# Optimization experiments

Measured on AMD Instinct MI355X. Metric: run time of the kernel, lower is better.

Reference implementation:

```python
import jax, jax.numpy as jnp
import numpy as np


def setup_inputs() -> dict:
    key = jax.random.key(0)
    kx, kb, kc, ka, kd = jax.random.split(key, 5)
    B, L, D, N = 8, 4096, 1024, 128
    x = jax.random.normal(kx, (B, L, D), jnp.float32)
    B_w = jax.random.normal(kb, (N, D), jnp.float32) * 0.01  # nn.Linear(d_model->d_state).weight
    C_w = jax.random.normal(kc, (D, N), jnp.float32)         # nn.Linear(d_state->d_model).weight
    # stable negative log_A (HiPPO init gives -|diag|+0.1 < 0)
    log_A = -jax.random.uniform(ka, (N,), jnp.float32) * 3.0 - 0.1
    D_param = jax.random.normal(kd, (D,), jnp.float32)
    return dict(x=x, B_w=B_w, C_w=C_w, log_A=log_A, D_param=D_param)


def reference(x, B_w, C_w, log_A, D_param):
    # x: (B,L,D); B_w: (N,D); C_w: (D,N); log_A: (N,); D_param: (D,)
    A = jnp.exp(log_A)                                   # (N,) diagonal transition
    x_proj = jnp.einsum('bld,nd->bln', x, B_w)           # B @ x  -> (B,L,N)

    def step(h, u):                                      # h_t = A*h_{t-1} + u_t
        h = A * h + u
        return h, h

    h0 = jnp.zeros((x.shape[0], B_w.shape[0]), x.dtype)  # (B,N)
    _, hs = jax.lax.scan(step, h0, jnp.swapaxes(x_proj, 0, 1))  # hs: (L,B,N)

    y = jnp.einsum('lbn,dn->bld', hs, C_w)               # C @ h -> (B,L,D)
    y = y + x * D_param                                  # skip term D*x

    last = x_proj[:, -1, :]                              # (B,N)
    final_state = jnp.broadcast_to(last.mean(axis=0, keepdims=True), last.shape)
    return y, final_state
```

## Files before the change

### kernel.cpp

```cpp
#include <hip/hip_runtime.h>


typedef _Float16 half8 __attribute__((ext_vector_type(8)));
typedef float f32x4 __attribute__((ext_vector_type(4)));

#define BDIM 8
#define LDIM 4096
#define DDIM 1024
#define NDIM 128
#define MTOT (BDIM * LDIM)
#define CHUNK 128
#define NCHUNK (LDIM / CHUNK)
#define TOTCHUNK (BDIM * NCHUNK)

__global__ __launch_bounds__(256) void gemm1(const float* __restrict__ x,
                                             const float* __restrict__ Bw,
                                             float* __restrict__ xp) {
    __shared__ _Float16 As[128 * 32];
    __shared__ _Float16 Bs[128 * 32];
    const int t = threadIdx.x;
    const int row0 = blockIdx.x * 128;
    const int wave = t >> 6, lane = t & 63;
    const int wr = (wave >> 1) * 64, wc = (wave & 1) * 64;
    const int lrow = lane & 15, kq = (lane >> 4) * 8;

    f32x4 acc[4][4] = {};

    for (int kk = 0; kk < 1024; kk += 32) {
#pragma unroll
        for (int j = 0; j < 4; ++j) {
            int i = t + 256 * j;
            int r = i >> 3, c4 = i & 7;
            float4 v = *reinterpret_cast<const float4*>(&x[(row0 + r) * 1024 + kk + c4 * 4]);
            _Float16* dst = &As[r * 32 + c4 * 4];
            dst[0] = (_Float16)v.x; dst[1] = (_Float16)v.y;
            dst[2] = (_Float16)v.z; dst[3] = (_Float16)v.w;
        }
#pragma unroll
        for (int j = 0; j < 4; ++j) {
            int i = t + 256 * j;
            int r = i >> 3, c4 = i & 7;
            float4 v = *reinterpret_cast<const float4*>(&Bw[r * 1024 + kk + c4 * 4]);
            _Float16* dst = &Bs[r * 32 + c4 * 4];
            dst[0] = (_Float16)v.x; dst[1] = (_Float16)v.y;
            dst[2] = (_Float16)v.z; dst[3] = (_Float16)v.w;
        }
        __syncthreads();

        half8 bf[4];
#pragma unroll
        for (int ct = 0; ct < 4; ++ct)
            bf[ct] = *reinterpret_cast<const half8*>(&Bs[(wc + ct * 16 + lrow) * 32 + kq]);
#pragma unroll
        for (int rt = 0; rt < 4; ++rt) {
            half8 af = *reinterpret_cast<const half8*>(&As[(wr + rt * 16 + lrow) * 32 + kq]);
#pragma unroll
            for (int ct = 0; ct < 4; ++ct)
                acc[rt][ct] = __builtin_amdgcn_mfma_f32_16x16x32_f16(af, bf[ct], acc[rt][ct], 0, 0, 0);
        }
        __syncthreads();
    }

    const int q4 = (lane >> 4) * 4;
#pragma unroll
    for (int rt = 0; rt < 4; ++rt) {
#pragma unroll
        for (int ct = 0; ct < 4; ++ct) {
            int col = wc + ct * 16 + lrow;
#pragma unroll
            for (int i = 0; i < 4; ++i)
                xp[(row0 + wr + rt * 16 + q4 + i) * 128 + col] = acc[rt][ct][i];
        }
    }
}

__global__ void scan_agg(const float* __restrict__ xp, const float* __restrict__ logA,
                         float* __restrict__ agg) {
    const int chunk = blockIdx.x;
    const int n = threadIdx.x;
    const float A = expf(logA[n]);
    const float* u = xp + chunk * CHUNK * 128 + n;
    float h = 0.f;
#pragma unroll 4
    for (int j = 0; j < CHUNK; ++j)
        h = fmaf(A, h, u[j * 128]);
    agg[chunk * 128 + n] = h;
}

__global__ void scan_carry(const float* __restrict__ agg, const float* __restrict__ logA,
                           float* __restrict__ hprev) {
    const int idx = blockIdx.x * blockDim.x + threadIdx.x;
    const int b = idx >> 7, n = idx & 127;
    const float A128 = expf(128.f * logA[n]);
    float c = 0.f;
    for (int ch = 0; ch < NCHUNK; ++ch) {
        int g = (b * NCHUNK + ch) * 128 + n;
        hprev[g] = c;
        c = fmaf(A128, c, agg[g]);
    }
}

__global__ void scan_final(const float* __restrict__ xp, const float* __restrict__ logA,
                           const float* __restrict__ hprev, _Float16* __restrict__ hs) {
    const int chunk = blockIdx.x;
    const int n = threadIdx.x;
    const float A = expf(logA[n]);
    float h = hprev[chunk * 128 + n];
    const float* u = xp + chunk * CHUNK * 128 + n;
    _Float16* o = hs + chunk * CHUNK * 128 + n;
#pragma unroll 4
    for (int j = 0; j < CHUNK; ++j) {
        h = fmaf(A, h, u[j * 128]);
        o[j * 128] = (_Float16)h;
    }
}

__global__ __launch_bounds__(256) void gemm2(const _Float16* __restrict__ hs,
                                             const float* __restrict__ Cw,
                                             const float* __restrict__ x,
                                             const float* __restrict__ Dp,
                                             float* __restrict__ y) {
    __shared__ _Float16 As[128 * 32];
    __shared__ _Float16 Bs[128 * 32];
    const int t = threadIdx.x;
    const int row0 = blockIdx.x * 128;
    const int col0 = blockIdx.y * 128;
    const int wave = t >> 6, lane = t & 63;
    const int wr = (wave >> 1) * 64, wc = (wave & 1) * 64;
    const int lrow = lane & 15, kq = (lane >> 4) * 8;

    f32x4 acc[4][4] = {};

    for (int kk = 0; kk < 128; kk += 32) {
#pragma unroll
        for (int j = 0; j < 2; ++j) {
            int i = t + 256 * j;
            int r = i >> 2, c8 = i & 3;
            *reinterpret_cast<half8*>(&As[r * 32 + c8 * 8]) =
                *reinterpret_cast<const half8*>(&hs[(row0 + r) * 128 + kk + c8 * 8]);
        }
#pragma unroll
        for (int j = 0; j < 4; ++j) {
            int i = t + 256 * j;
            int r = i >> 3, c4 = i & 7;
            float4 v = *reinterpret_cast<const float4*>(&Cw[(col0 + r) * 128 + kk + c4 * 4]);
            _Float16* dst = &Bs[r * 32 + c4 * 4];
            dst[0] = (_Float16)v.x; dst[1] = (_Float16)v.y;
            dst[2] = (_Float16)v.z; dst[3] = (_Float16)v.w;
        }
        __syncthreads();

        half8 bf[4];
#pragma unroll
        for (int ct = 0; ct < 4; ++ct)
            bf[ct] = *reinterpret_cast<const half8*>(&Bs[(wc + ct * 16 + lrow) * 32 + kq]);
#pragma unroll
        for (int rt = 0; rt < 4; ++rt) {
            half8 af = *reinterpret_cast<const half8*>(&As[(wr + rt * 16 + lrow) * 32 + kq]);
#pragma unroll
            for (int ct = 0; ct < 4; ++ct)
                acc[rt][ct] = __builtin_amdgcn_mfma_f32_16x16x32_f16(af, bf[ct], acc[rt][ct], 0, 0, 0);
        }
        __syncthreads();
    }

    const int q4 = (lane >> 4) * 4;
#pragma unroll
    for (int rt = 0; rt < 4; ++rt) {
#pragma unroll
        for (int ct = 0; ct < 4; ++ct) {
            int col = col0 + wc + ct * 16 + lrow;
            float dpv = Dp[col];
#pragma unroll
            for (int i = 0; i < 4; ++i) {
                int row = row0 + wr + rt * 16 + q4 + i;
                y[row * 1024 + col] = acc[rt][ct][i] + x[row * 1024 + col] * dpv;
            }
        }
    }
}

__global__ __launch_bounds__(256) void final_state_k(const float* __restrict__ x,
                                                     const float* __restrict__ Bw,
                                                     float* __restrict__ out) {
    const int n = blockIdx.x;
    const int t = threadIdx.x;
    float s = 0.f;
    for (int b = 0; b < BDIM; ++b) {
        const float* xr = x + ((size_t)b * LDIM + (LDIM - 1)) * DDIM;
        const float* br = Bw + n * DDIM;
        for (int k = t; k < DDIM; k += 256)
            s = fmaf(xr[k], br[k], s);
    }
    __shared__ float red[256];
    red[t] = s;
    __syncthreads();
    for (int off = 128; off > 0; off >>= 1) {
        if (t < off) red[t] += red[t + off];
        __syncthreads();
    }
    if (t == 0) {
        float v = red[0] * 0.125f;
        for (int b = 0; b < BDIM; ++b)
            out[(size_t)MTOT * DDIM + b * NDIM + n] = v;
    }
}

extern "C" void kernel_launch(void* const* d_in, const int* in_sizes, int n_in,
                              void* d_out, int out_size, void* d_ws, size_t ws_size,
                              hipStream_t stream) {
    const float* x    = (const float*)d_in[0];
    const float* Bw   = (const float*)d_in[1];
    const float* Cw   = (const float*)d_in[2];
    const float* logA = (const float*)d_in[3];
    const float* Dp   = (const float*)d_in[4];
    float* out = (float*)d_out;

    char* ws = (char*)d_ws;
    float*    xp    = (float*)   (ws);
    _Float16* hs    = (_Float16*)(ws + 16777216);
    float*    agg   = (float*)   (ws + 16777216 + 8388608);
    float*    hprev = (float*)   (ws + 16777216 + 8388608 + 131072);

    gemm1<<<MTOT / 128, 256, 0, stream>>>(x, Bw, xp);
    scan_agg<<<TOTCHUNK, 128, 0, stream>>>(xp, logA, agg);
    scan_carry<<<4, 256, 0, stream>>>(agg, logA, hprev);
    scan_final<<<TOTCHUNK, 128, 0, stream>>>(xp, logA, hprev, hs);
    gemm2<<<dim3(MTOT / 128, DDIM / 128), 256, 0, stream>>>(hs, Cw, x, Dp, out);
    final_state_k<<<NDIM, 256, 0, stream>>>(x, Bw, out);
}
```

Baseline: 402.0 us.

## Pre-convert weights to fp16, DMA tiles into LDS, coalesce gemm2 epilogue via LDS

Result: faster. 329.7 us (-18.0%).

```diff
diff --git a/kernel.cpp b/kernel.cpp
--- a/kernel.cpp
+++ b/kernel.cpp
@@ -2,6 +2,7 @@
 
 
 typedef _Float16 half8 __attribute__((ext_vector_type(8)));
+typedef _Float16 half4 __attribute__((ext_vector_type(4)));
 typedef float f32x4 __attribute__((ext_vector_type(4)));
 
 #define BDIM 8
@@ -13,37 +14,83 @@
 #define NCHUNK (LDIM / CHUNK)
 #define TOTCHUNK (BDIM * NCHUNK)
 
+__device__ __forceinline__ void dma16(const void* g, void* l) {
+    __builtin_amdgcn_global_load_lds((const __attribute__((address_space(1))) void*)g,
+                                     (__attribute__((address_space(3))) void*)l, 16, 0, 0);
+}
+
+__global__ __launch_bounds__(256) void prep(const float* __restrict__ x,
+                                            const float* __restrict__ Bw,
+                                            const float* __restrict__ Cw,
+                                            _Float16* __restrict__ Bwh,
+                                            _Float16* __restrict__ Cwh,
+                                            float* __restrict__ out) {
+    const int blk = blockIdx.x;
+    const int t = threadIdx.x;
+    if (blk < 128) {
+        const int n = blk;
+        float s = 0.f;
+        const float* br = Bw + n * DDIM;
+        for (int b = 0; b < BDIM; ++b) {
+            const float* xr = x + ((size_t)b * LDIM + (LDIM - 1)) * DDIM;
+            for (int k = t; k < DDIM; k += 256)
+                s = fmaf(xr[k], br[k], s);
+        }
+        __shared__ float red[256];
+        red[t] = s;
+        __syncthreads();
+        for (int off = 128; off > 0; off >>= 1) {
+            if (t < off) red[t] += red[t + off];
+            __syncthreads();
+        }
+        if (t == 0) {
+            float v = red[0] * 0.125f;
+            for (int b = 0; b < BDIM; ++b)
+                out[(size_t)MTOT * DDIM + b * NDIM + n] = v;
+        }
+    } else {
+        const int base = (blk - 128) * 4096;
+#pragma unroll
+        for (int j = 0; j < 4; ++j) {
+            int e = base + j * 1024 + t * 4;
+            const float* src;
+            _Float16* dst;
+            if (e < 131072) { src = Bw + e; dst = Bwh + e; }
+            else            { src = Cw + (e - 131072); dst = Cwh + (e - 131072); }
+            float4 v = *reinterpret_cast<const float4*>(src);
+            half4 h = { (_Float16)v.x, (_Float16)v.y, (_Float16)v.z, (_Float16)v.w };
+            *reinterpret_cast<half4*>(dst) = h;
+        }
+    }
+}
+
 __global__ __launch_bounds__(256) void gemm1(const float* __restrict__ x,
-                                             const float* __restrict__ Bw,
+                                             const _Float16* __restrict__ Bwh,
                                              float* __restrict__ xp) {
-    __shared__ _Float16 As[128 * 32];
+    __shared__ _Float16 As[64 * 32];
     __shared__ _Float16 Bs[128 * 32];
     const int t = threadIdx.x;
-    const int row0 = blockIdx.x * 128;
+    const int row0 = blockIdx.x * 64;
     const int wave = t >> 6, lane = t & 63;
-    const int wr = (wave >> 1) * 64, wc = (wave & 1) * 64;
+    const int wr = (wave >> 1) * 32, wc = (wave & 1) * 64;
     const int lrow = lane & 15, kq = (lane >> 4) * 8;
 
-    f32x4 acc[4][4] = {};
-
-    for (int kk = 0; kk < 1024; kk += 32) {
-#pragma unroll
-        for (int j = 0; j < 4; ++j) {
+    f32x4 acc[2][4] = {};
+
+    for (int kk = 0; kk < DDIM; kk += 32) {
+#pragma unroll
+        for (int j = 0; j < 2; ++j) {
             int i = t + 256 * j;
             int r = i >> 3, c4 = i & 7;
-            float4 v = *reinterpret_cast<const float4*>(&x[(row0 + r) * 1024 + kk + c4 * 4]);
-            _Float16* dst = &As[r * 32 + c4 * 4];
-            dst[0] = (_Float16)v.x; dst[1] = (_Float16)v.y;
-            dst[2] = (_Float16)v.z; dst[3] = (_Float16)v.w;
-        }
-#pragma unroll
-        for (int j = 0; j < 4; ++j) {
-            int i = t + 256 * j;
-            int r = i >> 3, c4 = i & 7;
-            float4 v = *reinterpret_cast<const float4*>(&Bw[r * 1024 + kk + c4 * 4]);
-            _Float16* dst = &Bs[r * 32 + c4 * 4];
-            dst[0] = (_Float16)v.x; dst[1] = (_Float16)v.y;
-            dst[2] = (_Float16)v.z; dst[3] = (_Float16)v.w;
+            float4 v = *reinterpret_cast<const float4*>(&x[(row0 + r) * DDIM + kk + c4 * 4]);
+            half4 h = { (_Float16)v.x, (_Float16)v.y, (_Float16)v.z, (_Float16)v.w };
+            *reinterpret_cast<half4*>(&As[r * 32 + c4 * 4]) = h;
+        }
+#pragma unroll
+        for (int inst = 0; inst < 2; ++inst) {
+            int s = inst * 256 + t;
+            int r = s >> 2, c8 = s & 3;
+            dma16(&Bwh[r * DDIM + kk + c8 * 8], &Bs[(inst * 256 + wave * 64) * 8]);
         }
         __syncthreads();
 
@@ -52,7 +99,7 @@
         for (int ct = 0; ct < 4; ++ct)
             bf[ct] = *reinterpret_cast<const half8*>(&Bs[(wc + ct * 16 + lrow) * 32 + kq]);
 #pragma unroll
-        for (int rt = 0; rt < 4; ++rt) {
+        for (int rt = 0; rt < 2; ++rt) {
             half8 af = *reinterpret_cast<const half8*>(&As[(wr + rt * 16 + lrow) * 32 + kq]);
 #pragma unroll
             for (int ct = 0; ct < 4; ++ct)
@@ -63,15 +110,14 @@
 
     const int q4 = (lane >> 4) * 4;
 #pragma unroll
-    for (int rt = 0; rt < 4; ++rt) {
+    for (int rt = 0; rt < 2; ++rt)
 #pragma unroll
         for (int ct = 0; ct < 4; ++ct) {
             int col = wc + ct * 16 + lrow;
 #pragma unroll
             for (int i = 0; i < 4; ++i)
-                xp[(row0 + wr + rt * 16 + q4 + i) * 128 + col] = acc[rt][ct][i];
-        }
-    }
+                xp[(row0 + wr + rt * 16 + q4 + i) * NDIM + col] = acc[rt][ct][i];
+        }
 }
 
 __global__ void scan_agg(const float* __restrict__ xp, const float* __restrict__ logA,
@@ -79,12 +125,12 @@
     const int chunk = blockIdx.x;
     const int n = threadIdx.x;
     const float A = expf(logA[n]);
-    const float* u = xp + chunk * CHUNK * 128 + n;
+    const float* u = xp + chunk * CHUNK * NDIM + n;
     float h = 0.f;
 #pragma unroll 4
     for (int j = 0; j < CHUNK; ++j)
-        h = fmaf(A, h, u[j * 128]);
-    agg[chunk * 128 + n] = h;
+        h = fmaf(A, h, u[j * NDIM]);
+    agg[chunk * NDIM + n] = h;
 }
 
 __global__ void scan_carry(const float* __restrict__ agg, const float* __restrict__ logA,
@@ -94,7 +140,7 @@
     const float A128 = expf(128.f * logA[n]);
     float c = 0.f;
     for (int ch = 0; ch < NCHUNK; ++ch) {
-        int g = (b * NCHUNK + ch) * 128 + n;
+        int g = (b * NCHUNK + ch) * NDIM + n;
         hprev[g] = c;
         c = fmaf(A128, c, agg[g]);
     }
@@ -105,23 +151,27 @@
     const int chunk = blockIdx.x;
     const int n = threadIdx.x;
     const float A = expf(logA[n]);
-    float h = hprev[chunk * 128 + n];
-    const float* u = xp + chunk * CHUNK * 128 + n;
-    _Float16* o = hs + chunk * CHUNK * 128 + n;
+    float h = hprev[chunk * NDIM + n];
+    const float* u = xp + chunk * CHUNK * NDIM + n;
+    _Float16* o = hs + chunk * CHUNK * NDIM + n;
 #pragma unroll 4
     for (int j = 0; j < CHUNK; ++j) {
-        h = fmaf(A, h, u[j * 128]);
-        o[j * 128] = (_Float16)h;
-    }
-}
-
+        h = fmaf(A, h, u[j * NDIM]);
+        o[j * NDIM] = (_Float16)h;
+    }
+}
+
+#define BUFW 132
 __global__ __launch_bounds__(256) void gemm2(const _Float16* __restrict__ hs,
-                                             const float* __restrict__ Cw,
+                                             const _Float16* __restrict__ Cwh,
                                              const float* __restrict__ x,
                                              const float* __restrict__ Dp,
                                              float* __restrict__ y) {
-    __shared__ _Float16 As[128 * 32];
-    __shared__ _Float16 Bs[128 * 32];
+    __shared__ char smem[65536];
+    __shared__ __align__(16) float DpS[128];
+    _Float16* hsP = (_Float16*)smem;
+    _Float16* CsP = (_Float16*)(smem + 32768);
+
     const int t = threadIdx.x;
     const int row0 = blockIdx.x * 128;
     const int col0 = blockIdx.y * 128;
@@ -129,80 +179,72 @@
     const int wr = (wave >> 1) * 64, wc = (wave & 1) * 64;
     const int lrow = lane & 15, kq = (lane >> 4) * 8;
 
+    if (t < 128) DpS[t] = Dp[col0 + t];
+
+#pragma unroll
+    for (int inst = 0; inst < 8; ++inst) {
+        int s = inst * 256 + t;
+        int kb = s >> 9, r = (s & 511) >> 2, c8 = s & 3;
+        void* ldst = &hsP[(inst * 256 + wave * 64) * 8];
+        dma16(&hs[(row0 + r) * NDIM + kb * 32 + c8 * 8], ldst);
+    }
+#pragma unroll
+    for (int inst = 0; inst < 8; ++inst) {
+        int s = inst * 256 + t;
+        int kb = s >> 9, r = (s & 511) >> 2, c8 = s & 3;
+        void* ldst = &CsP[(inst * 256 + wave * 64) * 8];
+        dma16(&Cwh[(col0 + r) * NDIM + kb * 32 + c8 * 8], ldst);
+    }
+    __syncthreads();
+
     f32x4 acc[4][4] = {};
-
-    for (int kk = 0; kk < 128; kk += 32) {
-#pragma unroll
-        for (int j = 0; j < 2; ++j) {
-            int i = t + 256 * j;
-            int r = i >> 2, c8 = i & 3;
-            *reinterpret_cast<half8*>(&As[r * 32 + c8 * 8]) =
-                *reinterpret_cast<const half8*>(&hs[(row0 + r) * 128 + kk + c8 * 8]);
-        }
-#pragma unroll
-        for (int j = 0; j < 4; ++j) {
-            int i = t + 256 * j;
-            int r = i >> 3, c4 = i & 7;
-            float4 v = *reinterpret_cast<const float4*>(&Cw[(col0 + r) * 128 + kk + c4 * 4]);
-            _Float16* dst = &Bs[r * 32 + c4 * 4];
-            dst[0] = (_Float16)v.x; dst[1] = (_Float16)v.y;
-            dst[2] = (_Float16)v.z; dst[3] = (_Float16)v.w;
-        }
-        __syncthreads();
-
+#pragma unroll
+    for (int kb = 0; kb < 4; ++kb) {
         half8 bf[4];
 #pragma unroll
         for (int ct = 0; ct < 4; ++ct)
-            bf[ct] = *reinterpret_cast<const half8*>(&Bs[(wc + ct * 16 + lrow) * 32 + kq]);
+            bf[ct] = *reinterpret_cast<const half8*>(&CsP[kb * 4096 + (wc + ct * 16 + lrow) * 32 + kq]);
 #pragma unroll
         for (int rt = 0; rt < 4; ++rt) {
-            half8 af = *reinterpret_cast<const half8*>(&As[(wr + rt * 16 + lrow) * 32 + kq]);
+            half8 af = *reinterpret_cast<const half8*>(&hsP[kb * 4096 + (wr + rt * 16 + lrow) * 32 + kq]);
 #pragma unroll
             for (int ct = 0; ct < 4; ++ct)
                 acc[rt][ct] = __builtin_amdgcn_mfma_f32_16x16x32_f16(af, bf[ct], acc[rt][ct], 0, 0, 0);
         }
-        __syncthreads();
-    }
-
+    }
+
+    float* buf = (float*)smem;
     const int q4 = (lane >> 4) * 4;
 #pragma unroll
-    for (int rt = 0; rt < 4; ++rt) {
-#pragma unroll
-        for (int ct = 0; ct < 4; ++ct) {
-            int col = col0 + wc + ct * 16 + lrow;
-            float dpv = Dp[col];
-#pragma unroll
-            for (int i = 0; i < 4; ++i) {
-                int row = row0 + wr + rt * 16 + q4 + i;
-                y[row * 1024 + col] = acc[rt][ct][i] + x[row * 1024 + col] * dpv;
-            }
-        }
-    }
-}
-
-__global__ __launch_bounds__(256) void final_state_k(const float* __restrict__ x,
-                                                     const float* __restrict__ Bw,
-                                                     float* __restrict__ out) {
-    const int n = blockIdx.x;
-    const int t = threadIdx.x;
-    float s = 0.f;
-    for (int b = 0; b < BDIM; ++b) {
-        const float* xr = x + ((size_t)b * LDIM + (LDIM - 1)) * DDIM;
-        const float* br = Bw + n * DDIM;
-        for (int k = t; k < DDIM; k += 256)
-            s = fmaf(xr[k], br[k], s);
-    }
-    __shared__ float red[256];
-    red[t] = s;
-    __syncthreads();
-    for (int off = 128; off > 0; off >>= 1) {
-        if (t < off) red[t] += red[t + off];
-        __syncthreads();
-    }
-    if (t == 0) {
-        float v = red[0] * 0.125f;
-        for (int b = 0; b < BDIM; ++b)
-            out[(size_t)MTOT * DDIM + b * NDIM + n] = v;
+    for (int half_ = 0; half_ < 2; ++half_) {
+        __syncthreads();
+        if ((wr >> 6) == half_) {
+#pragma unroll
+            for (int rt = 0; rt < 4; ++rt)
+#pragma unroll
+                for (int ct = 0; ct < 4; ++ct) {
+                    int col = wc + ct * 16 + lrow;
+#pragma unroll
+                    for (int i = 0; i < 4; ++i)
+                        buf[(rt * 16 + q4 + i) * BUFW + col] = acc[rt][ct][i];
+                }
+        }
+        __syncthreads();
+#pragma unroll
+        for (int j = 0; j < 8; ++j) {
+            int idx = t + 256 * j;
+            int row = idx >> 5, c4 = idx & 31;
+            int grow = row0 + half_ * 64 + row;
+            float4 a = *reinterpret_cast<const float4*>(&buf[row * BUFW + c4 * 4]);
+            float4 xv = *reinterpret_cast<const float4*>(&x[(size_t)grow * DDIM + col0 + c4 * 4]);
+            float4 dp = *reinterpret_cast<const float4*>(&DpS[c4 * 4]);
+            float4 o;
+            o.x = a.x + xv.x * dp.x;
+            o.y = a.y + xv.y * dp.y;
+            o.z = a.z + xv.z * dp.z;
+            o.w = a.w + xv.w * dp.w;
+            *reinterpret_cast<float4*>(&y[(size_t)grow * DDIM + col0 + c4 * 4]) = o;
+        }
     }
 }
 
@@ -219,13 +261,15 @@
     char* ws = (char*)d_ws;
     float*    xp    = (float*)   (ws);
     _Float16* hs    = (_Float16*)(ws + 16777216);
-    float*    agg   = (float*)   (ws + 16777216 + 8388608);
-    float*    hprev = (float*)   (ws + 16777216 + 8388608 + 131072);
-
-    gemm1<<<MTOT / 128, 256, 0, stream>>>(x, Bw, xp);
+    float*    agg   = (float*)   (ws + 25165824);
+    float*    hprev = (float*)   (ws + 25296896);
+    _Float16* Bwh   = (_Float16*)(ws + 25427968);
+    _Float16* Cwh   = (_Float16*)(ws + 25690112);
+
+    prep<<<192, 256, 0, stream>>>(x, Bw, Cw, Bwh, Cwh, out);
+    gemm1<<<MTOT / 64, 256, 0, stream>>>(x, Bwh, xp);
     scan_agg<<<TOTCHUNK, 128, 0, stream>>>(xp, logA, agg);
     scan_carry<<<4, 256, 0, stream>>>(agg, logA, hprev);
     scan_final<<<TOTCHUNK, 128, 0, stream>>>(xp, logA, hprev, hs);
-    gemm2<<<dim3(MTOT / 128, DDIM / 128), 256, 0, stream>>>(hs, Cw, x, Dp, out);
-    final_state_k<<<NDIM, 256, 0, stream>>>(x, Bw, out);
-}
+    gemm2<<<dim3(MTOT / 128, DDIM / 128), 256, 0, stream>>>(hs, Cwh, x, Dp, out);
+}
```
